# Optimization experiments

Hardware: AMD Instinct MI355X
Metric: run time of the kernel (lower is better)

Reference implementation:

```python
import jax, jax.numpy as jnp
import numpy as np

IN_DIM, HIDDEN, NCLASS = 128, 512, 10
BETA, THRESH = 0.9, 0.15


def setup_inputs() -> dict:
    key = jax.random.key(0)
    k_x, k_w1, k_w2 = jax.random.split(key, 3)
    B, T = 512, 512
    x = jax.random.uniform(k_x, (B, T, IN_DIM), dtype=jnp.float32)
    # kaiming_normal_(nonlinearity='linear'): std = 1/sqrt(fan_in); fc1 then scaled by 0.8
    W1 = jax.random.normal(k_w1, (HIDDEN, IN_DIM), dtype=jnp.float32) * (0.8 / np.sqrt(IN_DIM))
    b1 = jnp.zeros((HIDDEN,), dtype=jnp.float32)
    W2 = jax.random.normal(k_w2, (NCLASS, HIDDEN), dtype=jnp.float32) * (1.0 / np.sqrt(HIDDEN))
    b2 = jnp.zeros((NCLASS,), dtype=jnp.float32)
    return {"x": x, "W1": W1, "b1": b1, "W2": W2, "b2": b2}


def reference(x, W1, b1, W2, b2):
    B, T, D = x.shape
    xs = jnp.transpose(2.0 * x, (1, 0, 2))  # [T, B, D]

    def step(carry, xt):
        mem, acc = carry
        cur = xt @ W1.T + b1                      # [B, H]
        reset = (mem > THRESH).astype(cur.dtype)  # spike from previous mem (snntorch order)
        mem = BETA * mem + cur - reset * THRESH   # subtract reset
        spk = (mem > THRESH).astype(cur.dtype)
        acc = acc + spk @ W2.T + b2               # [B, C]
        return (mem, acc), None

    mem0 = jnp.zeros((B, HIDDEN), dtype=jnp.float32)
    acc0 = jnp.zeros((B, NCLASS), dtype=jnp.float32)
    (_, acc), _ = jax.lax.scan(step, (mem0, acc0), xs)
    return acc / T
```

## Files before the change

kernel.cpp:

```cpp
#include <hip/hip_runtime.h>

#define IN_DIM  128
#define HIDDEN  512
#define NCLASS  10
#define TSTEPS  512
#define BATCH   512
#define BETA    0.9f
#define THRESH  0.15f

typedef __attribute__((ext_vector_type(8))) short bf16x8;
typedef __attribute__((ext_vector_type(4))) float f32x4;

__device__ __forceinline__ unsigned short f2bf_rne(float f) {
    unsigned int u = __float_as_uint(f);
    u += 0x7FFFu + ((u >> 16) & 1u);
    return (unsigned short)(u >> 16);
}
__device__ __forceinline__ float bf2f(unsigned short h) {
    return __uint_as_float(((unsigned int)h) << 16);
}

__device__ __forceinline__ bf16x8 cvt8(const float4 a, const float4 b, float s) {
    float v[8] = {a.x * s, a.y * s, a.z * s, a.w * s,
                  b.x * s, b.y * s, b.z * s, b.w * s};
    bf16x8 o;
#pragma unroll
    for (int e = 0; e < 8; ++e) o[e] = (short)f2bf_rne(v[e]);
    return o;
}

__device__ __forceinline__ void cvt8s(const float4 a, const float4 b,
                                      bf16x8* hi, bf16x8* lo) {
    float v[8] = {a.x, a.y, a.z, a.w, b.x, b.y, b.z, b.w};
#pragma unroll
    for (int e = 0; e < 8; ++e) {
        unsigned short h = f2bf_rne(v[e]);
        (*hi)[e] = (short)h;
        (*lo)[e] = (short)f2bf_rne(v[e] - bf2f(h));
    }
}

__global__ __launch_bounds__(256, 4) void conv_x3(
    const float* __restrict__ x, unsigned short* __restrict__ xt)
{
    const int bid  = blockIdx.x;
    const int bblk = bid >> 9;
    const int t    = bid & 511;
    const int g    = threadIdx.x;
    const int kf   = g >> 6;
    const int i    = g & 63;
    const int l15  = i & 15;
    const int lg   = i >> 4;

    const float* src = x + ((size_t)(bblk * 16 + l15) * TSTEPS + t) * IN_DIM
                         + kf * 32 + lg * 8;
    const float4* p = reinterpret_cast<const float4*>(src);
    unsigned short* tile = xt + ((size_t)bblk * TSTEPS + t) * 2048;
    *(bf16x8*)(tile + g * 8) = cvt8(p[0], p[1], 2.0f);
}

__global__ __launch_bounds__(256, 1) void snn_mfma_a(
    const unsigned short* __restrict__ xt,
    const float* __restrict__ W1, const float* __restrict__ b1,
    float* __restrict__ cnt_ws)
{
    __shared__ char ring[16][4096];

    const int bid  = blockIdx.x;
    const int hblk = bid >> 5;
    const int bblk = bid & 31;
    const int b0   = bblk * 16;
    const int tid  = threadIdx.x;
    const int wave = tid >> 6;
    const int lane = tid & 63;
    const int l15  = lane & 15;
    const int lg   = lane >> 4;
    const int hbase = hblk * 64 + wave * 16;

    bf16x8 whi[4], wlo[4];
    {
        const float* wp = W1 + (size_t)(hbase + l15) * IN_DIM + lg * 8;
#pragma unroll
        for (int kf = 0; kf < 4; ++kf) {
            const float4* p = reinterpret_cast<const float4*>(wp + kf * 32);
            cvt8s(p[0], p[1], &whi[kf], &wlo[kf]);
        }
    }
    const float b1h = b1[hbase + l15];
    const f32x4 B1 = {b1h, b1h, b1h, b1h};
    const f32x4 Z0 = {0.f, 0.f, 0.f, 0.f};

    const char* gb = (const char*)xt + (size_t)bblk * TSTEPS * 4096;
    char* lsb = &ring[0][0];
    const int woff   = wave * 1024;
    const int lane16 = lane * 16;
    const unsigned lbase =
        (unsigned)(unsigned long long)(__attribute__((address_space(3))) char*)&ring[0][0]
        + (unsigned)lane16;

    f32x4 mem = {0.f, 0.f, 0.f, 0.f}, cnt = {0.f, 0.f, 0.f, 0.f};

#define STAGE(TT)                                                              \
    {                                                                          \
        const char* g_ = gb + (size_t)(TT) * 4096 + woff + lane16;             \
        char* l_ = lsb + ((TT) & 15) * 4096 + woff;                            \
        __builtin_amdgcn_global_load_lds((const __attribute__((address_space(1))) void*)g_, (__attribute__((address_space(3))) void*)l_, 16, 0, 0); \
    }

#define RD1(OFF, DST)                                                          \
    asm volatile("ds_read_b128 %0, %1 offset:%c2"                              \
                 : "=&v"(DST) : "v"(lbase), "i"(OFF))

#define RD4A(S, F)                                                             \
    RD1((S) * 4096 + 0,    F[0]);                                              \
    RD1((S) * 4096 + 1024, F[1]);                                              \
    RD1((S) * 4096 + 2048, F[2]);                                              \
    RD1((S) * 4096 + 3072, F[3]);

#define MFMA_PAIR(F0, F1, H0, L0, H1, L1)                                      \
    H0 = __builtin_amdgcn_mfma_f32_16x16x32_bf16(F0[0], whi[0], B1, 0, 0, 0);  \
    H1 = __builtin_amdgcn_mfma_f32_16x16x32_bf16(F1[0], whi[0], B1, 0, 0, 0);  \
    L0 = __builtin_amdgcn_mfma_f32_16x16x32_bf16(F0[0], wlo[0], Z0, 0, 0, 0);  \
    L1 = __builtin_amdgcn_mfma_f32_16x16x32_bf16(F1[0], wlo[0], Z0, 0, 0, 0);  \
    _Pragma("unroll")                                                          \
    for (int kf = 1; kf < 4; ++kf) {                                           \
        H0 = __builtin_amdgcn_mfma_f32_16x16x32_bf16(F0[kf], whi[kf], H0, 0, 0, 0); \
        H1 = __builtin_amdgcn_mfma_f32_16x16x32_bf16(F1[kf], whi[kf], H1, 0, 0, 0); \
        L0 = __builtin_amdgcn_mfma_f32_16x16x32_bf16(F0[kf], wlo[kf], L0, 0, 0, 0); \
        L1 = __builtin_amdgcn_mfma_f32_16x16x32_bf16(F1[kf], wlo[kf], L1, 0, 0, 0); \
    }

#define REC(PH, PL)                                                            \
    _Pragma("unroll")                                                          \
    for (int r = 0; r < 4; ++r) {                                              \
        float cur = PH[r] + PL[r];                                             \
        float dec = fmaf(BETA, mem[r], cur);                                   \
        mem[r] = (mem[r] > THRESH) ? (dec - THRESH) : dec;                     \
        cnt[r] += (mem[r] > THRESH) ? 1.0f : 0.0f;                             \
    }

#define PAIR_B(J, CF0, CF1, NF0, NF1)                                          \
    {                                                                          \
        asm volatile("s_waitcnt vmcnt(2)" ::: "memory");                       \
        __builtin_amdgcn_s_barrier();                                          \
        asm volatile("" ::: "memory");                                         \
        STAGE(tb + 2 * (J) + 8)                                                \
        STAGE(tb + 2 * (J) + 9)                                                \
        RD4A((tb + 2 * (J) + 2) & 15, NF0)                                     \
        RD4A((tb + 2 * (J) + 3) & 15, NF1)                                     \
        asm volatile("s_waitcnt lgkmcnt(8)" ::: "memory");                     \
        __builtin_amdgcn_sched_barrier(0);                                     \
        MFMA_PAIR(CF0, CF1, hA, lA, hB, lB)                                    \
        REC(hA, lA)                                                            \
        REC(hB, lB)                                                            \
    }

#define PAIR_N(J, CF0, CF1, NF0, NF1)                                          \
    {                                                                          \
        STAGE(tb + 2 * (J) + 8)                                                \
        STAGE(tb + 2 * (J) + 9)                                                \
        RD4A((tb + 2 * (J) + 2) & 15, NF0)                                     \
        RD4A((tb + 2 * (J) + 3) & 15, NF1)                                     \
        asm volatile("s_waitcnt lgkmcnt(8)" ::: "memory");                     \
        __builtin_amdgcn_sched_barrier(0);                                     \
        MFMA_PAIR(CF0, CF1, hA, lA, hB, lB)                                    \
        REC(hA, lA)                                                            \
        REC(hB, lB)                                                            \
    }

    bf16x8 fA[4], fB[4], fC[4], fD[4];
    f32x4 hA, lA, hB, lB;

    asm volatile("s_waitcnt vmcnt(0)" ::: "memory");
#pragma unroll
    for (int j = 0; j < 8; ++j)
        STAGE(j)
    asm volatile("s_waitcnt vmcnt(6)" ::: "memory");
    __builtin_amdgcn_s_barrier();
    asm volatile("" ::: "memory");
    RD4A(0, fA)
    RD4A(1, fB)

    for (int w = 0; w < TSTEPS / 16; ++w) {
        const int tb = w * 16;
        PAIR_B(0, fA, fB, fC, fD)  PAIR_N(1, fC, fD, fA, fB)
        PAIR_B(2, fA, fB, fC, fD)  PAIR_N(3, fC, fD, fA, fB)
        PAIR_B(4, fA, fB, fC, fD)  PAIR_N(5, fC, fD, fA, fB)
        PAIR_B(6, fA, fB, fC, fD)  PAIR_N(7, fC, fD, fA, fB)
    }
#undef PAIR_B
#undef PAIR_N
#undef REC
#undef MFMA_PAIR
#undef RD4A
#undef RD1
#undef STAGE

    float* cp = cnt_ws + (size_t)b0 * HIDDEN + hbase + l15;
#pragma unroll
    for (int r = 0; r < 4; ++r)
        cp[(size_t)(lg * 4 + r) * HIDDEN] = cnt[r];
}

__global__ __launch_bounds__(256, 1) void snn_mfma_lds(
    const float* __restrict__ x, const float* __restrict__ W1,
    const float* __restrict__ b1, float* __restrict__ cnt_ws)
{
    __shared__ short ldsA[2][2][16 * IN_DIM];
    const int bid  = blockIdx.x;
    const int hblk = bid >> 5;
    const int bblk = bid & 31;
    const int b0   = bblk * 16;
    const int tid  = threadIdx.x;
    const int wave = tid >> 6;
    const int lane = tid & 63;
    const int l15  = lane & 15;
    const int lg   = lane >> 4;
    const int hbase = hblk * 64 + wave * 16;

    bf16x8 whi[4], wlo[4];
    {
        const float* wp = W1 + (size_t)(hbase + l15) * IN_DIM + lg * 8;
#pragma unroll
        for (int kf = 0; kf < 4; ++kf) {
            const float4* p = reinterpret_cast<const float4*>(wp + kf * 32);
            cvt8s(p[0], p[1], &whi[kf], &wlo[kf]);
        }
    }
    const float b1h = b1[hbase + l15];
    const int m_w  = wave * 4 + lg;
    const int widx = m_w * IN_DIM + ((l15 ^ (m_w & 7)) * 8);
    const float* xrow = x + ((size_t)(b0 + m_w) * TSTEPS) * IN_DIM + l15 * 8;
    int ridx[4];
#pragma unroll
    for (int kf = 0; kf < 4; ++kf)
        ridx[kf] = l15 * IN_DIM + (((lg + 4 * kf) ^ (l15 & 7)) * 8);

    f32x4 mem = {0.f, 0.f, 0.f, 0.f};
    f32x4 cnt = {0.f, 0.f, 0.f, 0.f};
    {
        const float4* p = reinterpret_cast<const float4*>(xrow);
        *(bf16x8*)&ldsA[0][0][widx] = cvt8(p[0], p[1], 2.0f);
    }
    float4 rA0, rA1, rB0, rB1;
    {
        const float4* p1 = reinterpret_cast<const float4*>(xrow + 1 * IN_DIM);
        rA0 = p1[0]; rA1 = p1[1];
        const float4* p2 = reinterpret_cast<const float4*>(xrow + 2 * IN_DIM);
        rB0 = p2[0]; rB1 = p2[1];
    }
    __syncthreads();

#define SNN_BODY(T_CUR, RC0, RC1)                                              \
    {                                                                          \
        const int buf = (T_CUR) & 1;                                           \
        if ((T_CUR) + 1 < TSTEPS) {                                            \
            *(bf16x8*)&ldsA[buf ^ 1][0][widx] = cvt8(RC0, RC1, 2.0f);          \
        }                                                                      \
        bf16x8 ahi[4];                                                         \
        _Pragma("unroll")                                                      \
        for (int kf = 0; kf < 4; ++kf)                                         \
            ahi[kf] = *(const bf16x8*)&ldsA[buf][0][ridx[kf]];                 \
        {                                                                      \
            int tld = (T_CUR) + 3;                                             \
            if (tld > TSTEPS - 1) tld = TSTEPS - 1;                            \
            const float4* p = reinterpret_cast<const float4*>(                 \
                xrow + (size_t)tld * IN_DIM);                                  \
            RC0 = p[0]; RC1 = p[1];                                            \
        }                                                                      \
        f32x4 chh = {b1h, b1h, b1h, b1h};                                      \
        f32x4 chl = {0.f, 0.f, 0.f, 0.f};                                      \
        _Pragma("unroll")                                                      \
        for (int kf = 0; kf < 4; ++kf) {                                       \
            chh = __builtin_amdgcn_mfma_f32_16x16x32_bf16(ahi[kf], whi[kf], chh, 0, 0, 0); \
            chl = __builtin_amdgcn_mfma_f32_16x16x32_bf16(ahi[kf], wlo[kf], chl, 0, 0, 0); \
        }                                                                      \
        _Pragma("unroll")                                                      \
        for (int r = 0; r < 4; ++r) {                                          \
            float cur = chh[r] + chl[r];                                       \
            float dec = fmaf(BETA, mem[r], cur);                               \
            mem[r] = (mem[r] > THRESH) ? (dec - THRESH) : dec;                 \
            cnt[r] += (mem[r] > THRESH) ? 1.0f : 0.0f;                         \
        }                                                                      \
        __syncthreads();                                                       \
    }

    for (int t = 0; t < TSTEPS; t += 2) {
        SNN_BODY(t,     rA0, rA1)
        SNN_BODY(t + 1, rB0, rB1)
    }
#undef SNN_BODY

    float* cp = cnt_ws + (size_t)b0 * HIDDEN + hbase + l15;
#pragma unroll
    for (int r = 0; r < 4; ++r)
        cp[(size_t)(lg * 4 + r) * HIDDEN] = cnt[r];
}

__global__ __launch_bounds__(64, 1) void snn_out(
    const float* __restrict__ cnt_ws, const float* __restrict__ W2,
    const float* __restrict__ b2, float* __restrict__ out)
{
    const int b = blockIdx.x;
    const int lane = threadIdx.x;
    float c8[8];
#pragma unroll
    for (int j = 0; j < 8; ++j)
        c8[j] = cnt_ws[(size_t)b * HIDDEN + lane + 64 * j];
#pragma unroll
    for (int c = 0; c < NCLASS; ++c) {
        float s = 0.f;
#pragma unroll
        for (int j = 0; j < 8; ++j)
            s = fmaf(c8[j], W2[c * HIDDEN + lane + 64 * j], s);
#pragma unroll
        for (int off = 32; off >= 1; off >>= 1)
            s += __shfl_xor(s, off, 64);
        if (lane == c)
            out[(size_t)b * NCLASS + c] = s * (1.0f / (float)TSTEPS) + b2[c];
    }
}

extern "C" void kernel_launch(void* const* d_in, const int* in_sizes, int n_in,
                              void* d_out, int out_size, void* d_ws, size_t ws_size,
                              hipStream_t stream) {
    const float* x  = (const float*)d_in[0];
    const float* W1 = (const float*)d_in[1];
    const float* b1 = (const float*)d_in[2];
    const float* W2 = (const float*)d_in[3];
    const float* b2 = (const float*)d_in[4];
    float* out = (float*)d_out;

    const size_t NX = (size_t)BATCH * TSTEPS * IN_DIM;
    float* cnt_ws = (float*)d_ws;
    unsigned short* xt = (unsigned short*)((char*)d_ws + (1u << 20));
    const size_t need = (1u << 20) + (NX + 8 * 2048) * sizeof(unsigned short);

    if (ws_size >= need) {
        conv_x3<<<dim3(32 * TSTEPS), dim3(256), 0, stream>>>(x, xt);
        snn_mfma_a<<<dim3(256), dim3(256), 0, stream>>>(xt, W1, b1, cnt_ws);
    } else {
        snn_mfma_lds<<<dim3(256), dim3(256), 0, stream>>>(x, W1, b1, cnt_ws);
    }
    snn_out<<<dim3(BATCH), dim3(64), 0, stream>>>(cnt_ws, W2, b2, out);
}
```

Baseline: 116.8 us.

## Load x tiles straight to registers with deep prefetch, dropping LDS ring and barriers

Replaces the global_load_lds staging ring and ds_read path with direct global_load_dwordx4 into a register ring of eight timestep fragments, kept six steps ahead. Waits use vmcnt counts instead of per-pair workgroup barriers. The aim is to remove LDS round-trips and barrier stalls from the serial recurrence. In exchange each wave now fetches the full tile itself, so global/L2 traffic per block is roughly four times higher and register pressure rises. The prefetch also reads past the last timestep of each batch block.

Result: faster. 113.5 us (-2.9%).

```diff
diff --git a/kernel.cpp b/kernel.cpp
--- a/kernel.cpp
+++ b/kernel.cpp
@@ -64,8 +64,6 @@
     const float* __restrict__ W1, const float* __restrict__ b1,
     float* __restrict__ cnt_ws)
 {
-    __shared__ char ring[16][4096];
-
     const int bid  = blockIdx.x;
     const int hblk = bid >> 5;
     const int bblk = bid & 31;
@@ -90,32 +88,18 @@
     const f32x4 B1 = {b1h, b1h, b1h, b1h};
     const f32x4 Z0 = {0.f, 0.f, 0.f, 0.f};
 
-    const char* gb = (const char*)xt + (size_t)bblk * TSTEPS * 4096;
-    char* lsb = &ring[0][0];
-    const int woff   = wave * 1024;
-    const int lane16 = lane * 16;
-    const unsigned lbase =
-        (unsigned)(unsigned long long)(__attribute__((address_space(3))) char*)&ring[0][0]
-        + (unsigned)lane16;
+    const unsigned short* gbase = xt + (size_t)bblk * TSTEPS * 2048;
+    unsigned voff = (unsigned)(lane * 16);
 
     f32x4 mem = {0.f, 0.f, 0.f, 0.f}, cnt = {0.f, 0.f, 0.f, 0.f};
 
-#define STAGE(TT)                                                              \
-    {                                                                          \
-        const char* g_ = gb + (size_t)(TT) * 4096 + woff + lane16;             \
-        char* l_ = lsb + ((TT) & 15) * 4096 + woff;                            \
-        __builtin_amdgcn_global_load_lds((const __attribute__((address_space(1))) void*)g_, (__attribute__((address_space(3))) void*)l_, 16, 0, 0); \
-    }
-
-#define RD1(OFF, DST)                                                          \
-    asm volatile("ds_read_b128 %0, %1 offset:%c2"                              \
-                 : "=&v"(DST) : "v"(lbase), "i"(OFF))
-
-#define RD4A(S, F)                                                             \
-    RD1((S) * 4096 + 0,    F[0]);                                              \
-    RD1((S) * 4096 + 1024, F[1]);                                              \
-    RD1((S) * 4096 + 2048, F[2]);                                              \
-    RD1((S) * 4096 + 3072, F[3]);
+#define GLD(IMM, DST)                                                          \
+    asm volatile("global_load_dwordx4 %0, %1, %2 offset:%c3"                   \
+                 : "=&v"(DST) : "v"(voff), "s"(gbase), "i"(IMM))
+
+#define STG(F)                                                                 \
+    GLD(0, F[0]); GLD(1024, F[1]); GLD(2048, F[2]); GLD(3072, F[3]);           \
+    voff += 4096;
 
 #define MFMA_PAIR(F0, F1, H0, L0, H1, L1)                                      \
     H0 = __builtin_amdgcn_mfma_f32_16x16x32_bf16(F0[0], whi[0], B1, 0, 0, 0);  \
@@ -139,62 +123,34 @@
         cnt[r] += (mem[r] > THRESH) ? 1.0f : 0.0f;                             \
     }
 
-#define PAIR_B(J, CF0, CF1, NF0, NF1)                                          \
+#define PAIR(C0, C1, N0, N1)                                                   \
     {                                                                          \
-        asm volatile("s_waitcnt vmcnt(2)" ::: "memory");                       \
-        __builtin_amdgcn_s_barrier();                                          \
-        asm volatile("" ::: "memory");                                         \
-        STAGE(tb + 2 * (J) + 8)                                                \
-        STAGE(tb + 2 * (J) + 9)                                                \
-        RD4A((tb + 2 * (J) + 2) & 15, NF0)                                     \
-        RD4A((tb + 2 * (J) + 3) & 15, NF1)                                     \
-        asm volatile("s_waitcnt lgkmcnt(8)" ::: "memory");                     \
+        STG(N0)                                                                \
+        STG(N1)                                                                \
+        asm volatile("s_waitcnt vmcnt(24)" ::: "memory");                      \
         __builtin_amdgcn_sched_barrier(0);                                     \
-        MFMA_PAIR(CF0, CF1, hA, lA, hB, lB)                                    \
+        MFMA_PAIR(C0, C1, hA, lA, hB, lB)                                      \
         REC(hA, lA)                                                            \
         REC(hB, lB)                                                            \
     }
 
-#define PAIR_N(J, CF0, CF1, NF0, NF1)                                          \
-    {                                                                          \
-        STAGE(tb + 2 * (J) + 8)                                                \
-        STAGE(tb + 2 * (J) + 9)                                                \
-        RD4A((tb + 2 * (J) + 2) & 15, NF0)                                     \
-        RD4A((tb + 2 * (J) + 3) & 15, NF1)                                     \
-        asm volatile("s_waitcnt lgkmcnt(8)" ::: "memory");                     \
-        __builtin_amdgcn_sched_barrier(0);                                     \
-        MFMA_PAIR(CF0, CF1, hA, lA, hB, lB)                                    \
-        REC(hA, lA)                                                            \
-        REC(hB, lB)                                                            \
-    }
-
-    bf16x8 fA[4], fB[4], fC[4], fD[4];
+    bf16x8 s0[4], s1[4], s2[4], s3[4], s4[4], s5[4], s6[4], s7[4];
     f32x4 hA, lA, hB, lB;
 
     asm volatile("s_waitcnt vmcnt(0)" ::: "memory");
-#pragma unroll
-    for (int j = 0; j < 8; ++j)
-        STAGE(j)
-    asm volatile("s_waitcnt vmcnt(6)" ::: "memory");
-    __builtin_amdgcn_s_barrier();
-    asm volatile("" ::: "memory");
-    RD4A(0, fA)
-    RD4A(1, fB)
-
-    for (int w = 0; w < TSTEPS / 16; ++w) {
-        const int tb = w * 16;
-        PAIR_B(0, fA, fB, fC, fD)  PAIR_N(1, fC, fD, fA, fB)
-        PAIR_B(2, fA, fB, fC, fD)  PAIR_N(3, fC, fD, fA, fB)
-        PAIR_B(4, fA, fB, fC, fD)  PAIR_N(5, fC, fD, fA, fB)
-        PAIR_B(6, fA, fB, fC, fD)  PAIR_N(7, fC, fD, fA, fB)
-    }
-#undef PAIR_B
-#undef PAIR_N
+    STG(s0) STG(s1) STG(s2) STG(s3) STG(s4) STG(s5)
+
+    for (int w = 0; w < TSTEPS / 8; ++w) {
+        PAIR(s0, s1, s6, s7)
+        PAIR(s2, s3, s0, s1)
+        PAIR(s4, s5, s2, s3)
+        PAIR(s6, s7, s4, s5)
+    }
+#undef PAIR
 #undef REC
 #undef MFMA_PAIR
-#undef RD4A
-#undef RD1
-#undef STAGE
+#undef STG
+#undef GLD
 
     float* cp = cnt_ws + (size_t)b0 * HIDDEN + hbase + l15;
 #pragma unroll
```
